# Optimization experiments

Hardware: AMD Instinct MI355X
Metric: run time of the kernel (lower is better)

Reference implementation:

```python
import jax, jax.numpy as jnp
import numpy as np

N, E, K, IN, OUT = 20000, 320000, 5, 256, 128
NAN_FRAC = 0.3


def setup_inputs() -> dict:
    key = jax.random.key(0)
    ks = jax.random.split(key, 8)
    x = jax.random.normal(ks[0], (N, IN), dtype=jnp.float32)
    nan_mask = jax.random.uniform(ks[1], (N, IN)) < NAN_FRAC
    x = jnp.where(nan_mask, jnp.nan, x)  # missing features as NaN
    edge_index = jax.random.randint(ks[2], (2, E), 0, N, dtype=jnp.int64)
    logp = jax.nn.log_softmax(jax.random.normal(ks[3], (K,), dtype=jnp.float32))
    means = jax.random.normal(ks[4], (K, IN), dtype=jnp.float32)
    logvars = jax.random.normal(ks[5], (K, IN), dtype=jnp.float32) * 0.1
    xav = 1.414 * np.sqrt(6.0 / (IN + OUT))
    weight = jax.random.uniform(ks[6], (IN, OUT), dtype=jnp.float32, minval=-xav, maxval=xav)
    bias = jnp.zeros((OUT,), dtype=jnp.float32)
    return {"x": x, "edge_index": edge_index, "logp": logp, "means": means,
            "logvars": logvars, "weight": weight, "bias": bias}


def _ex_relu(mu, sigma):
    # E[relu(X)] for X ~ N(mu, sigma); sigma is the variance
    sigma_s = jnp.where(sigma == 0, 1e-10, sigma)
    ss = jnp.sqrt(sigma_s)
    w = mu / ss
    nr = ss * (jnp.exp(-0.5 * w * w) / np.sqrt(2 * np.pi)
               + 0.5 * w * (1.0 + jax.lax.erf(w / np.sqrt(2))))
    return jnp.where(sigma == 0, jnp.maximum(mu, 0.0), nr)


def _gcn_norm(edge_index, num_nodes):
    # add self-loops, symmetric D^-1/2 A D^-1/2 normalization
    row = jnp.concatenate([edge_index[0], jnp.arange(num_nodes, dtype=edge_index.dtype)])
    col = jnp.concatenate([edge_index[1], jnp.arange(num_nodes, dtype=edge_index.dtype)])
    ones = jnp.ones(row.shape[0], dtype=jnp.float32)
    deg = jax.ops.segment_sum(ones, row, num_segments=num_nodes)
    dinv = jnp.where(deg > 0, jax.lax.rsqrt(deg), 0.0)
    wn = dinv[row] * dinv[col]
    return row, col, wn


def reference(x, edge_index, logp, means, logvars, weight, bias):
    n = x.shape[0]
    dim = x.shape[1]
    row, col, wn = _gcn_norm(edge_index, n)
    wn2 = wn * wn  # adj2 = adj * adj (elementwise on sparse values)

    isnan = jnp.isnan(x)                                       # [N, IN]
    variances = jnp.exp(logvars)                               # [K, IN]
    mean_mat = jnp.where(isnan[None], means[:, None, :], x[None])      # [K, N, IN]
    var_mat = jnp.where(isnan[None], variances[:, None, :], 0.0)       # [K, N, IN]

    transform_x = jnp.einsum('kni,io->kno', mean_mat, weight) + bias   # [K, N, OUT]
    transform_covs = jnp.einsum('kni,io->kno', var_mat, weight * weight)

    def spmm(vals, X):  # segment-sum SpMM: out[r] += vals_e * X[c]
        return jax.ops.segment_sum(X[col] * vals[:, None], row, num_segments=n)

    conv_x = jax.vmap(lambda X: spmm(wn, X))(transform_x)      # [K, N, OUT]
    conv_covs = jax.vmap(lambda X: spmm(wn2, X))(transform_covs)

    expected_x = _ex_relu(conv_x, conv_covs)                   # [K, N, OUT]

    # GMM responsibilities per node
    log_n = (-0.5 * jnp.sum((mean_mat - means[:, None, :]) ** 2 / variances[:, None, :], axis=2)
             - 0.5 * dim * np.log(2 * np.pi) - 0.5 * jnp.sum(logvars))  # [K, N]
    gamma = jax.nn.softmax(logp[:, None] + log_n, axis=0)      # [K, N]

    return jnp.sum(expected_x * gamma[:, :, None], axis=0)     # [N, OUT]
```

## Files before the change

kernel.cpp:

```cpp
#include <hip/hip_runtime.h>
#include <stdint.h>

#define N_NODES 20000
#define N_EDGES 320000
#define K_MIX 5
#define IN_F 256
#define OUT_F 128
#define NT 11

typedef __attribute__((ext_vector_type(8))) short short8;
typedef __attribute__((ext_vector_type(4))) float floatx4;

__device__ __forceinline__ float bf2f(unsigned int u) {
  union { unsigned int i; float f; } v;
  v.i = (u & 0xffffu) << 16;
  return v.f;
}
__device__ __forceinline__ unsigned short f2bf(float f) {
  union { float f; unsigned int i; } v;
  v.f = f;
  unsigned int x = v.i;
  unsigned int r = (x + 0x7fffu + ((x >> 16) & 1u)) >> 16;
  return (unsigned short)r;
}

__device__ __forceinline__ float exrelu(float mu, float sig) {
  if (sig < 1e-30f) return fmaxf(mu, 0.f);
  float ss = sqrtf(sig);
  float w = mu / ss;
  float e = __expf(-0.5f * w * w);
  float axv = fabsf(w) * 0.70710678118654752f;
  float t = 1.f / (1.f + 0.3275911f * axv);
  float poly = t * (0.254829592f +
              t * (-0.284496736f +
              t * (1.421413741f +
              t * (-1.453152027f + t * 1.061405429f))));
  float erfv = 1.f - poly * e;
  erfv = copysignf(erfv, w);
  return ss * (e * 0.3989422804014327f + 0.5f * w * (1.f + erfv));
}

__global__ void k_deg(const int* __restrict__ row, int* __restrict__ deg) {
  int t = blockIdx.x * 256 + threadIdx.x;
  if (t < N_EDGES) atomicAdd(&deg[row[t]], 1);
}

__global__ void k_scan1(const int* __restrict__ deg, int* __restrict__ startofs,
                        int* __restrict__ bsums, float* __restrict__ dinv) {
  __shared__ int sd[256];
  int t = threadIdx.x;
  int i = blockIdx.x * 256 + t;
  int v = (i < N_NODES) ? deg[i] : 0;
  if (i < N_NODES) dinv[i] = rsqrtf((float)(v + 1));
  sd[t] = v;
  __syncthreads();
  for (int off = 1; off < 256; off <<= 1) {
    int u = (t >= off) ? sd[t - off] : 0;
    __syncthreads();
    sd[t] += u;
    __syncthreads();
  }
  if (i < N_NODES) startofs[i] = sd[t] - v;
  if (t == 255) bsums[blockIdx.x] = sd[255];
}

__global__ void k_scan2(int* __restrict__ bsums, int nb) {
  __shared__ int sd[128];
  int t = threadIdx.x;
  int v = (t < nb) ? bsums[t] : 0;
  sd[t] = v;
  __syncthreads();
  for (int off = 1; off < 128; off <<= 1) {
    int u = (t >= off) ? sd[t - off] : 0;
    __syncthreads();
    sd[t] += u;
    __syncthreads();
  }
  if (t < nb) bsums[t] = sd[t] - v;
}

__global__ void k_scan3(int* __restrict__ startofs, int* __restrict__ cursor,
                        const int* __restrict__ bsums) {
  int i = blockIdx.x * 256 + threadIdx.x;
  if (i < N_NODES) {
    int s0 = startofs[i] + bsums[blockIdx.x];
    startofs[i] = s0;
    cursor[i] = s0;
  }
}

__global__ void k_scatter(const int* __restrict__ row, const int* __restrict__ col,
                          const float* __restrict__ dinv, int* __restrict__ cursor,
                          int* __restrict__ csr_col, float* __restrict__ csr_w) {
  int t = blockIdx.x * 256 + threadIdx.x;
  if (t < N_EDGES) {
    int r = row[t], c = col[t];
    int p = atomicAdd(&cursor[r], 1);
    csr_col[p] = c;
    csr_w[p] = dinv[r] * dinv[c];
  }
}

__global__ void k_buildB(const float* __restrict__ W, const float* __restrict__ means,
                         const float* __restrict__ logvars, unsigned short* __restrict__ Bt) {
  int idx = blockIdx.x * 256 + threadIdx.x;
  int j = idx >> 15;
  int rem = idx & 32767;
  int n = rem >> 8;
  int kk = rem & 255;
  float wv = W[kk * OUT_F + n];
  float val;
  if (j == 0) val = wv;
  else if (j <= 5) val = means[(j - 1) * IN_F + kk] * wv;
  else val = expf(logvars[(j - 6) * IN_F + kk]) * wv * wv;
  Bt[idx] = f2bf(val);
}

__global__ void k_prepx(const float* __restrict__ x, const float* __restrict__ logp,
                        const float* __restrict__ means, const float* __restrict__ logvars,
                        unsigned short* __restrict__ X0, float* __restrict__ gamma) {
  __shared__ float s_mean[K_MIX * IN_F];
  __shared__ float s_rv[K_MIX * IN_F];
  int t = threadIdx.x;
  for (int j = t; j < K_MIX * IN_F; j += 256) {
    s_mean[j] = means[j];
    s_rv[j] = expf(-logvars[j]);
  }
  __syncthreads();
  int node = blockIdx.x * 4 + (t >> 6);
  if (node >= N_NODES) return;
  int lane = t & 63;
  float4 xv = *(const float4*)(x + (size_t)node * IN_F + 4 * lane);
  float xf[4] = {xv.x, xv.y, xv.z, xv.w};
  float gsum[K_MIX] = {0, 0, 0, 0, 0};
  ushort4 o;
  unsigned short* op = (unsigned short*)&o;
#pragma unroll
  for (int j = 0; j < 4; j++) {
    bool nn = (xf[j] != xf[j]);
    op[j] = nn ? (unsigned short)0x7FC0 : f2bf(xf[j]);
    if (!nn) {
      int fi = 4 * lane + j;
#pragma unroll
      for (int k = 0; k < K_MIX; k++) {
        float d = xf[j] - s_mean[k * IN_F + fi];
        gsum[k] += d * d * s_rv[k * IN_F + fi];
      }
    }
  }
  *(ushort4*)(X0 + node * IN_F + 4 * lane) = o;
#pragma unroll
  for (int k = 0; k < K_MIX; k++)
    for (int off = 32; off; off >>= 1) gsum[k] += __shfl_xor(gsum[k], off, 64);
  if (lane == 0) {
    float lg[K_MIX], mx = -1e30f;
#pragma unroll
    for (int k = 0; k < K_MIX; k++) {
      lg[k] = logp[k] - 0.5f * gsum[k];
      mx = fmaxf(mx, lg[k]);
    }
    float se = 0.f;
#pragma unroll
    for (int k = 0; k < K_MIX; k++) { lg[k] = expf(lg[k] - mx); se += lg[k]; }
    float inv = 1.f / se;
#pragma unroll
    for (int k = 0; k < K_MIX; k++) gamma[node * K_MIX + k] = lg[k] * inv;
  }
}

__global__ __launch_bounds__(64) void k_spmm(const unsigned short* __restrict__ X0,
                       const int* __restrict__ startofs, const int* __restrict__ deg,
                       const float* __restrict__ dinv, const int* __restrict__ csr_col,
                       const float* __restrict__ csr_w, unsigned short* __restrict__ G,
                       float* __restrict__ sArr) {
  int node = blockIdx.x;
  int lane = threadIdx.x;
  int fo = 4 * lane;
  float ax[4] = {0, 0, 0, 0}, am[4] = {0, 0, 0, 0}, am2[4] = {0, 0, 0, 0};
  float ssum = 0.f;
  float ws = dinv[node];
  ws = ws * ws;
  int st = startofs[node];
  int total = deg[node] + 1;
  ushort4 zero4 = {0, 0, 0, 0};
  ushort4 B0 = zero4, B1 = zero4, B2 = zero4, B3 = zero4,
          B4 = zero4, B5 = zero4, B6 = zero4, B7 = zero4;
  float W0 = 0.f, W1 = 0.f, W2 = 0.f, W3 = 0.f,
        W4 = 0.f, W5 = 0.f, W6 = 0.f, W7 = 0.f;
  B0 = *(const ushort4*)(X0 + node * IN_F + fo); W0 = ws;
#define PFILL(S)                                                      \
  if (S < total) {                                                    \
    int c = csr_col[st + (S - 1)];                                    \
    W##S = csr_w[st + (S - 1)];                                       \
    B##S = *(const ushort4*)(X0 + c * IN_F + fo);                     \
  }
  PFILL(1) PFILL(2) PFILL(3) PFILL(4) PFILL(5) PFILL(6) PFILL(7)
#undef PFILL

#define STEP(S)                                                       \
  if (W##S != 0.f) {                                                  \
    float wv = W##S, wv2 = wv * wv;                                   \
    ssum += wv;                                                       \
    const unsigned short* xp = (const unsigned short*)&B##S;          \
    _Pragma("unroll")                                                 \
    for (int j = 0; j < 4; j++) {                                     \
      float xf = bf2f(xp[j]);                                         \
      bool nn = (xf != xf);                                           \
      ax[j] = fmaf(wv, nn ? 0.f : xf, ax[j]);                         \
      am[j] += nn ? wv : 0.f;                                         \
      am2[j] += nn ? wv2 : 0.f;                                       \
    }                                                                 \
  }                                                                   \
  if (base + 8 + S < total) {                                         \
    int c = csr_col[st + base + 7 + S];                               \
    W##S = csr_w[st + base + 7 + S];                                  \
    B##S = *(const ushort4*)(X0 + c * IN_F + fo);                     \
  } else {                                                            \
    W##S = 0.f;                                                       \
  }

  for (int base = 0; base < total; base += 8) {
    STEP(0) STEP(1) STEP(2) STEP(3) STEP(4) STEP(5) STEP(6) STEP(7)
  }
#undef STEP

  ushort4 o;
  o.x = f2bf(ax[0]); o.y = f2bf(ax[1]); o.z = f2bf(ax[2]); o.w = f2bf(ax[3]);
  *(ushort4*)(G + node * 768 + fo) = o;
  o.x = f2bf(am[0]); o.y = f2bf(am[1]); o.z = f2bf(am[2]); o.w = f2bf(am[3]);
  *(ushort4*)(G + node * 768 + 256 + fo) = o;
  o.x = f2bf(am2[0]); o.y = f2bf(am2[1]); o.z = f2bf(am2[2]); o.w = f2bf(am2[3]);
  *(ushort4*)(G + node * 768 + 512 + fo) = o;
  if (lane == 0) sArr[node] = ssum;
}

__global__ __launch_bounds__(256, 2) void k_gemm_ep(
    const unsigned short* __restrict__ G, const unsigned short* __restrict__ Bt,
    const float* __restrict__ gamma, const float* __restrict__ sArr,
    const float* __restrict__ bias, float* __restrict__ out) {
  __shared__ __align__(16) char A1ls[64 * 512];
  __shared__ __align__(16) char A2ls[64 * 512];
  __shared__ __align__(16) char Bls0[64 * 128];
  __shared__ __align__(16) char Bls1[64 * 128];
  int mt = blockIdx.x, ch = blockIdx.y;
  int t = threadIdx.x, wave = t >> 6, lane = t & 63;
  int wr = wave >> 1, wc = wave & 1;
  int quad = lane >> 4, l16 = lane & 15;

  floatx4 z = {0.f, 0.f, 0.f, 0.f};
  floatx4 cx[2][2], oa[2][2];
#pragma unroll
  for (int mi = 0; mi < 2; mi++)
#pragma unroll
    for (int ni = 0; ni < 2; ni++) { cx[mi][ni] = z; oa[mi][ni] = z; }

#define STAGE_A(dst, aoff_)                                              \
  {                                                                      \
    _Pragma("unroll")                                                    \
    for (int i = 0; i < 8; i++) {                                        \
      int f = i * 256 + t;                                               \
      int r = f >> 5, c = f & 31;                                        \
      int sw = c ^ (r & 7);                                              \
      int gr = mt * 64 + r;                                              \
      if (gr >= N_NODES) gr = N_NODES - 1;                               \
      *(uint4*)((dst) + r * 512 + sw * 16) =                             \
          *(const uint4*)(G + (size_t)gr * 768 + (aoff_) + c * 8);       \
    }                                                                    \
  }

#define STAGE_B(dst, jt_, k0_)                                           \
  {                                                                      \
    _Pragma("unroll")                                                    \
    for (int i = 0; i < 2; i++) {                                        \
      int f = i * 256 + t;                                               \
      int r = f >> 3, c = f & 7;                                         \
      int sw = c ^ (r & 7);                                              \
      *(uint4*)((dst) + r * 128 + sw * 16) =                             \
          *(const uint4*)(Bt + (size_t)(jt_)*32768 +                     \
                          (ch * 64 + r) * 256 + (k0_) + c * 8);          \
    }                                                                    \
  }

  STAGE_A(A1ls, 0)
  for (int k0 = 0; k0 < 256; k0 += 64) {
    __syncthreads();
    STAGE_B(Bls0, 0, k0)
    __syncthreads();
#pragma unroll
    for (int ks = 0; ks < 2; ks++) {
      int ccA = (k0 >> 3) + ks * 4 + quad;
      int ccB = ks * 4 + quad;
      short8 a[2], b[2];
#pragma unroll
      for (int mi = 0; mi < 2; mi++) {
        int r = wr * 32 + mi * 16 + l16;
        a[mi] = *(const short8*)(A1ls + r * 512 + (ccA ^ (r & 7)) * 16);
      }
#pragma unroll
      for (int ni = 0; ni < 2; ni++) {
        int r = wc * 32 + ni * 16 + l16;
        b[ni] = *(const short8*)(Bls0 + r * 128 + (ccB ^ (r & 7)) * 16);
      }
#pragma unroll
      for (int mi = 0; mi < 2; mi++)
#pragma unroll
        for (int ni = 0; ni < 2; ni++)
          cx[mi][ni] = __builtin_amdgcn_mfma_f32_16x16x32_bf16(a[mi], b[ni], cx[mi][ni], 0, 0, 0);
    }
  }

  __syncthreads();
  STAGE_A(A1ls, 256)
  STAGE_A(A2ls, 512)

  int gr0 = mt * 64 + wr * 32 + quad * 4;
  int gc0 = ch * 64 + wc * 32 + l16;
  float svr[2][4];
#pragma unroll
  for (int mi = 0; mi < 2; mi++)
#pragma unroll
    for (int reg = 0; reg < 4; reg++) {
      int gr = gr0 + mi * 16 + reg;
      if (gr >= N_NODES) gr = N_NODES - 1;
      svr[mi][reg] = sArr[gr];
    }
  float biasr[2] = {bias[gc0], bias[gc0 + 16]};

#pragma unroll 1
  for (int k = 0; k < K_MIX; k++) {
    floatx4 tm[2][2], tv[2][2];
#pragma unroll
    for (int mi = 0; mi < 2; mi++)
#pragma unroll
      for (int ni = 0; ni < 2; ni++) { tm[mi][ni] = z; tv[mi][ni] = z; }
    for (int k0 = 0; k0 < 256; k0 += 64) {
      __syncthreads();
      STAGE_B(Bls0, 1 + k, k0)
      STAGE_B(Bls1, 6 + k, k0)
      __syncthreads();
#pragma unroll
      for (int ks = 0; ks < 2; ks++) {
        int ccA = (k0 >> 3) + ks * 4 + quad;
        int ccB = ks * 4 + quad;
        short8 a1[2], a2[2], bm[2], bv[2];
#pragma unroll
        for (int mi = 0; mi < 2; mi++) {
          int r = wr * 32 + mi * 16 + l16;
          int sa = r * 512 + (ccA ^ (r & 7)) * 16;
          a1[mi] = *(const short8*)(A1ls + sa);
          a2[mi] = *(const short8*)(A2ls + sa);
        }
#pragma unroll
        for (int ni = 0; ni < 2; ni++) {
          int r = wc * 32 + ni * 16 + l16;
          int sb = r * 128 + (ccB ^ (r & 7)) * 16;
          bm[ni] = *(const short8*)(Bls0 + sb);
          bv[ni] = *(const short8*)(Bls1 + sb);
        }
#pragma unroll
        for (int mi = 0; mi < 2; mi++)
#pragma unroll
          for (int ni = 0; ni < 2; ni++) {
            tm[mi][ni] = __builtin_amdgcn_mfma_f32_16x16x32_bf16(a1[mi], bm[ni], tm[mi][ni], 0, 0, 0);
            tv[mi][ni] = __builtin_amdgcn_mfma_f32_16x16x32_bf16(a2[mi], bv[ni], tv[mi][ni], 0, 0, 0);
          }
      }
    }
#pragma unroll
    for (int mi = 0; mi < 2; mi++)
#pragma unroll
      for (int reg = 0; reg < 4; reg++) {
        int gr = gr0 + mi * 16 + reg;
        if (gr >= N_NODES) gr = N_NODES - 1;
        float g = gamma[gr * K_MIX + k];
#pragma unroll
        for (int ni = 0; ni < 2; ni++) {
          float mu = cx[mi][ni][reg] + tm[mi][ni][reg] + biasr[ni] * svr[mi][reg];
          oa[mi][ni][reg] += g * exrelu(mu, tv[mi][ni][reg]);
        }
      }
  }

#pragma unroll
  for (int mi = 0; mi < 2; mi++)
#pragma unroll
    for (int ni = 0; ni < 2; ni++)
#pragma unroll
      for (int reg = 0; reg < 4; reg++) {
        int gr = gr0 + mi * 16 + reg;
        if (gr < N_NODES) out[(size_t)gr * OUT_F + gc0 + ni * 16] = oa[mi][ni][reg];
      }
#undef STAGE_A
#undef STAGE_B
}

extern "C" void kernel_launch(void* const* d_in, const int* in_sizes, int n_in,
                              void* d_out, int out_size, void* d_ws, size_t ws_size,
                              hipStream_t stream) {
  const float* x = (const float*)d_in[0];
  const int* ei = (const int*)d_in[1];
  const float* logp = (const float*)d_in[2];
  const float* means = (const float*)d_in[3];
  const float* lvar = (const float*)d_in[4];
  const float* W = (const float*)d_in[5];
  const float* bias = (const float*)d_in[6];
  float* out = (float*)d_out;
  const int* row = ei;
  const int* col = ei + N_EDGES;

  char* p = (char*)d_ws;
  auto alloc = [&](size_t bytes) -> char* {
    char* q = p;
    p += (bytes + 255) & ~((size_t)255);
    return q;
  };
  int* deg = (int*)alloc(N_NODES * 4);
  float* dinv = (float*)alloc(N_NODES * 4);
  int* startofs = (int*)alloc(N_NODES * 4);
  int* cursor = (int*)alloc(N_NODES * 4);
  int* bsums = (int*)alloc(128 * 4);
  int* csr_col = (int*)alloc((size_t)N_EDGES * 4);
  float* csr_w = (float*)alloc((size_t)N_EDGES * 4);
  float* gamma = (float*)alloc((size_t)N_NODES * K_MIX * 4);
  float* sArr = (float*)alloc(N_NODES * 4);
  unsigned short* Bt = (unsigned short*)alloc((size_t)NT * 128 * 256 * 2);
  unsigned short* X0 = (unsigned short*)alloc((size_t)N_NODES * IN_F * 2);
  unsigned short* G = (unsigned short*)alloc((size_t)N_NODES * 768 * 2);

  hipMemsetAsync(deg, 0, N_NODES * 4, stream);
  k_deg<<<(N_EDGES + 255) / 256, 256, 0, stream>>>(row, deg);
  k_scan1<<<79, 256, 0, stream>>>(deg, startofs, bsums, dinv);
  k_scan2<<<1, 128, 0, stream>>>(bsums, 79);
  k_scan3<<<79, 256, 0, stream>>>(startofs, cursor, bsums);
  k_scatter<<<(N_EDGES + 255) / 256, 256, 0, stream>>>(row, col, dinv, cursor, csr_col, csr_w);
  k_buildB<<<(NT * 128 * 256) / 256, 256, 0, stream>>>(W, means, lvar, Bt);
  k_prepx<<<N_NODES / 4, 256, 0, stream>>>(x, logp, means, lvar, X0, gamma);
  k_spmm<<<N_NODES, 64, 0, stream>>>(X0, startofs, deg, dinv, csr_col, csr_w, G, sArr);
  k_gemm_ep<<<dim3((N_NODES + 63) / 64, 2), 256, 0, stream>>>(G, Bt, gamma, sArr, bias, out);
}
```

Before: 242.2 us.

## Pipeline GEMM B tiles via async global_load_lds into a triple-buffered ring

Rewrites the fused GEMM+epilogue kernel so all three A panels are staged up front using direct global-to-LDS loads, and B tiles flow through a 3-slot LDS ring prefetched with global_load_lds and gated by vmcnt waits. Gamma, scale and bias values are preloaded into shared memory once per block. This is meant to hide global memory latency behind MFMA work and remove the register round-trip of the old staging. In exchange LDS use rises to about 146KB, which likely cuts occupancy below the 2 blocks the launch bounds request. Correctness also depends on hand-tuned waitcnt counts.

New measurement: 284.8 us. +17.6%, slower.

```diff
diff --git a/kernel.cpp b/kernel.cpp
--- a/kernel.cpp
+++ b/kernel.cpp
@@ -38,6 +38,12 @@
   float erfv = 1.f - poly * e;
   erfv = copysignf(erfv, w);
   return ss * (e * 0.3989422804014327f + 0.5f * w * (1.f + erfv));
+}
+
+__device__ __forceinline__ void gll16(const void* g, void* l) {
+  __builtin_amdgcn_global_load_lds(
+      (const __attribute__((address_space(1))) void*)g,
+      (__attribute__((address_space(3))) void*)l, 16, 0, 0);
 }
 
 __global__ void k_deg(const int* __restrict__ row, int* __restrict__ deg) {
@@ -238,106 +244,120 @@
     const unsigned short* __restrict__ G, const unsigned short* __restrict__ Bt,
     const float* __restrict__ gamma, const float* __restrict__ sArr,
     const float* __restrict__ bias, float* __restrict__ out) {
-  __shared__ __align__(16) char A1ls[64 * 512];
-  __shared__ __align__(16) char A2ls[64 * 512];
-  __shared__ __align__(16) char Bls0[64 * 128];
-  __shared__ __align__(16) char Bls1[64 * 128];
+  __shared__ __align__(16) char A0ls[32768];
+  __shared__ __align__(16) char A1ls[32768];
+  __shared__ __align__(16) char A2ls[32768];
+  __shared__ __align__(16) char Bring[3 * 16384];
+  __shared__ float aux[448];
+
   int mt = blockIdx.x, ch = blockIdx.y;
-  int t = threadIdx.x, wave = t >> 6, lane = t & 63;
-  int wr = wave >> 1, wc = wave & 1;
-  int quad = lane >> 4, l16 = lane & 15;
+  int t = threadIdx.x, w = t >> 6, l = t & 63;
+  int wr = w >> 1, wc = w & 1;
+  int quad = l >> 4, l16 = l & 15;
+
+  for (int j = t; j < 448; j += 256) {
+    float v;
+    if (j < 320) {
+      int r = j / 5, k = j - r * 5;
+      int gr = mt * 64 + r; if (gr >= N_NODES) gr = N_NODES - 1;
+      v = gamma[gr * K_MIX + k];
+    } else if (j < 384) {
+      int gr = mt * 64 + (j - 320); if (gr >= N_NODES) gr = N_NODES - 1;
+      v = sArr[gr];
+    } else {
+      v = bias[ch * 64 + (j - 384)];
+    }
+    aux[j] = v;
+  }
+
+  {
+#pragma unroll
+    for (int s = 0; s < 3; s++) {
+      char* dst = (s == 0) ? A0ls : (s == 1) ? A1ls : A2ls;
+      int aoff = s * 256;
+#pragma unroll
+      for (int i = 0; i < 8; ++i) {
+        int r = i * 8 + w * 2 + (l >> 5);
+        int c = (l & 31) ^ (r & 7);
+        int gr = mt * 64 + r; if (gr >= N_NODES) gr = N_NODES - 1;
+        gll16(G + (size_t)gr * 768 + aoff + c * 8, dst + i * 4096 + w * 1024);
+      }
+    }
+  }
+
+#define ISSUE_B(qv, slotp)                                                \
+  {                                                                       \
+    int jm_, jv_, k0_;                                                    \
+    int q_ = (qv);                                                        \
+    if (q_ < 4) { jm_ = 0; jv_ = 0; k0_ = q_ * 64; }                      \
+    else { int qq_ = q_ - 4; int k_ = qq_ >> 2;                           \
+           jm_ = 1 + k_; jv_ = 6 + k_; k0_ = (qq_ & 3) * 64; }            \
+    int rb_ = w * 8 + (l >> 3);                                           \
+    int c8_ = ((l & 7) ^ ((l >> 3) & 7)) * 8;                             \
+    const unsigned short* bm_ =                                           \
+        Bt + jm_ * 32768 + (ch * 64 + rb_) * 256 + k0_ + c8_;             \
+    const unsigned short* bv_ =                                           \
+        Bt + jv_ * 32768 + (ch * 64 + rb_) * 256 + k0_ + c8_;             \
+    gll16(bm_, (slotp) + w * 1024);                                       \
+    gll16(bm_ + 32 * 256, (slotp) + 4096 + w * 1024);                     \
+    gll16(bv_, (slotp) + 8192 + w * 1024);                                \
+    gll16(bv_ + 32 * 256, (slotp) + 12288 + w * 1024);                    \
+  }
+
+  ISSUE_B(0, Bring)
+  ISSUE_B(1, Bring + 16384)
+  ISSUE_B(2, Bring + 32768)
+
+  asm volatile("s_waitcnt lgkmcnt(0)" ::: "memory");
 
   floatx4 z = {0.f, 0.f, 0.f, 0.f};
-  floatx4 cx[2][2], oa[2][2];
+  floatx4 cx[2][2], oa[2][2], tm[2][2], tv[2][2];
 #pragma unroll
   for (int mi = 0; mi < 2; mi++)
 #pragma unroll
     for (int ni = 0; ni < 2; ni++) { cx[mi][ni] = z; oa[mi][ni] = z; }
 
-#define STAGE_A(dst, aoff_)                                              \
-  {                                                                      \
-    _Pragma("unroll")                                                    \
-    for (int i = 0; i < 8; i++) {                                        \
-      int f = i * 256 + t;                                               \
-      int r = f >> 5, c = f & 31;                                        \
-      int sw = c ^ (r & 7);                                              \
-      int gr = mt * 64 + r;                                              \
-      if (gr >= N_NODES) gr = N_NODES - 1;                               \
-      *(uint4*)((dst) + r * 512 + sw * 16) =                             \
-          *(const uint4*)(G + (size_t)gr * 768 + (aoff_) + c * 8);       \
-    }                                                                    \
-  }
-
-#define STAGE_B(dst, jt_, k0_)                                           \
-  {                                                                      \
-    _Pragma("unroll")                                                    \
-    for (int i = 0; i < 2; i++) {                                        \
-      int f = i * 256 + t;                                               \
-      int r = f >> 3, c = f & 7;                                         \
-      int sw = c ^ (r & 7);                                              \
-      *(uint4*)((dst) + r * 128 + sw * 16) =                             \
-          *(const uint4*)(Bt + (size_t)(jt_)*32768 +                     \
-                          (ch * 64 + r) * 256 + (k0_) + c * 8);          \
-    }                                                                    \
-  }
-
-  STAGE_A(A1ls, 0)
-  for (int k0 = 0; k0 < 256; k0 += 64) {
-    __syncthreads();
-    STAGE_B(Bls0, 0, k0)
-    __syncthreads();
-#pragma unroll
-    for (int ks = 0; ks < 2; ks++) {
-      int ccA = (k0 >> 3) + ks * 4 + quad;
-      int ccB = ks * 4 + quad;
-      short8 a[2], b[2];
-#pragma unroll
-      for (int mi = 0; mi < 2; mi++) {
-        int r = wr * 32 + mi * 16 + l16;
-        a[mi] = *(const short8*)(A1ls + r * 512 + (ccA ^ (r & 7)) * 16);
-      }
-#pragma unroll
-      for (int ni = 0; ni < 2; ni++) {
-        int r = wc * 32 + ni * 16 + l16;
-        b[ni] = *(const short8*)(Bls0 + r * 128 + (ccB ^ (r & 7)) * 16);
-      }
-#pragma unroll
-      for (int mi = 0; mi < 2; mi++)
-#pragma unroll
-        for (int ni = 0; ni < 2; ni++)
-          cx[mi][ni] = __builtin_amdgcn_mfma_f32_16x16x32_bf16(a[mi], b[ni], cx[mi][ni], 0, 0, 0);
-    }
-  }
-
-  __syncthreads();
-  STAGE_A(A1ls, 256)
-  STAGE_A(A2ls, 512)
-
-  int gr0 = mt * 64 + wr * 32 + quad * 4;
-  int gc0 = ch * 64 + wc * 32 + l16;
-  float svr[2][4];
-#pragma unroll
-  for (int mi = 0; mi < 2; mi++)
-#pragma unroll
-    for (int reg = 0; reg < 4; reg++) {
-      int gr = gr0 + mi * 16 + reg;
-      if (gr >= N_NODES) gr = N_NODES - 1;
-      svr[mi][reg] = sArr[gr];
-    }
-  float biasr[2] = {bias[gc0], bias[gc0 + 16]};
-
-#pragma unroll 1
-  for (int k = 0; k < K_MIX; k++) {
-    floatx4 tm[2][2], tv[2][2];
-#pragma unroll
-    for (int mi = 0; mi < 2; mi++)
-#pragma unroll
-      for (int ni = 0; ni < 2; ni++) { tm[mi][ni] = z; tv[mi][ni] = z; }
-    for (int k0 = 0; k0 < 256; k0 += 64) {
-      __syncthreads();
-      STAGE_B(Bls0, 1 + k, k0)
-      STAGE_B(Bls1, 6 + k, k0)
-      __syncthreads();
+  for (int p = 0; p < 24; ++p) {
+    int sl = p - (p / 3) * 3;
+    char* slot = Bring + sl * 16384;
+
+    if (p < 22)       asm volatile("s_waitcnt vmcnt(8)" ::: "memory");
+    else if (p == 22) asm volatile("s_waitcnt vmcnt(4)" ::: "memory");
+    else              asm volatile("s_waitcnt vmcnt(0)" ::: "memory");
+    __builtin_amdgcn_s_barrier();
+
+    if (p < 4) {
+      int k0 = p * 64;
+#pragma unroll
+      for (int ks = 0; ks < 2; ks++) {
+        int ccA = (k0 >> 3) + ks * 4 + quad;
+        int ccB = ks * 4 + quad;
+        short8 a[2], b[2];
+#pragma unroll
+        for (int mi = 0; mi < 2; mi++) {
+          int r = wr * 32 + mi * 16 + l16;
+          a[mi] = *(const short8*)(A0ls + r * 512 + (ccA ^ (r & 7)) * 16);
+        }
+#pragma unroll
+        for (int ni = 0; ni < 2; ni++) {
+          int r = wc * 32 + ni * 16 + l16;
+          b[ni] = *(const short8*)(slot + r * 128 + (ccB ^ (r & 7)) * 16);
+        }
+#pragma unroll
+        for (int mi = 0; mi < 2; mi++)
+#pragma unroll
+          for (int ni = 0; ni < 2; ni++)
+            cx[mi][ni] = __builtin_amdgcn_mfma_f32_16x16x32_bf16(a[mi], b[ni], cx[mi][ni], 0, 0, 0);
+      }
+    } else {
+      int q = p - 4;
+      int k0 = (q & 3) * 64;
+      if ((q & 3) == 0) {
+#pragma unroll
+        for (int mi = 0; mi < 2; mi++)
+#pragma unroll
+          for (int ni = 0; ni < 2; ni++) { tm[mi][ni] = z; tv[mi][ni] = z; }
+      }
 #pragma unroll
       for (int ks = 0; ks < 2; ks++) {
         int ccA = (k0 >> 3) + ks * 4 + quad;
@@ -354,8 +374,8 @@
         for (int ni = 0; ni < 2; ni++) {
           int r = wc * 32 + ni * 16 + l16;
           int sb = r * 128 + (ccB ^ (r & 7)) * 16;
-          bm[ni] = *(const short8*)(Bls0 + sb);
-          bv[ni] = *(const short8*)(Bls1 + sb);
+          bm[ni] = *(const short8*)(slot + sb);
+          bv[ni] = *(const short8*)(slot + 8192 + sb);
         }
 #pragma unroll
         for (int mi = 0; mi < 2; mi++)
@@ -365,22 +385,35 @@
             tv[mi][ni] = __builtin_amdgcn_mfma_f32_16x16x32_bf16(a2[mi], bv[ni], tv[mi][ni], 0, 0, 0);
           }
       }
+      if ((q & 3) == 3) {
+        int kk = q >> 2;
+#pragma unroll
+        for (int mi = 0; mi < 2; mi++)
+#pragma unroll
+          for (int reg = 0; reg < 4; reg++) {
+            int row = wr * 32 + mi * 16 + quad * 4 + reg;
+            float g = aux[row * 5 + kk];
+            float sv = aux[320 + row];
+#pragma unroll
+            for (int ni = 0; ni < 2; ni++) {
+              float bia = aux[384 + wc * 32 + ni * 16 + l16];
+              float mu = cx[mi][ni][reg] + tm[mi][ni][reg] + bia * sv;
+              oa[mi][ni][reg] += g * exrelu(mu, tv[mi][ni][reg]);
+            }
+          }
+      }
     }
-#pragma unroll
-    for (int mi = 0; mi < 2; mi++)
-#pragma unroll
-      for (int reg = 0; reg < 4; reg++) {
-        int gr = gr0 + mi * 16 + reg;
-        if (gr >= N_NODES) gr = N_NODES - 1;
-        float g = gamma[gr * K_MIX + k];
-#pragma unroll
-        for (int ni = 0; ni < 2; ni++) {
-          float mu = cx[mi][ni][reg] + tm[mi][ni][reg] + biasr[ni] * svr[mi][reg];
-          oa[mi][ni][reg] += g * exrelu(mu, tv[mi][ni][reg]);
-        }
-      }
-  }
-
+
+    asm volatile("s_waitcnt lgkmcnt(0)" ::: "memory");
+    __builtin_amdgcn_s_barrier();
+    if (p + 3 < 24) ISSUE_B(p + 3, slot)
+  }
+#undef ISSUE_B
+
+  asm volatile("s_waitcnt vmcnt(0)" ::: "memory");
+
+  int gr0 = mt * 64 + wr * 32 + quad * 4;
+  int gc0 = ch * 64 + wc * 32 + l16;
 #pragma unroll
   for (int mi = 0; mi < 2; mi++)
 #pragma unroll
@@ -390,8 +423,6 @@
         int gr = gr0 + mi * 16 + reg;
         if (gr < N_NODES) out[(size_t)gr * OUT_F + gc0 + ni * 16] = oa[mi][ni][reg];
       }
-#undef STAGE_A
-#undef STAGE_B
 }
 
 extern "C" void kernel_launch(void* const* d_in, const int* in_sizes, int n_in,
```

## Load GEMM B fragments directly from global and stage A via global_load_lds

Applied to the files above, without the earlier changes.

The fused GEMM+epilogue kernel stops staging the weight (B) tiles through LDS and instead has each lane read its MFMA B fragment straight from global memory, which removes two barriers per k-step in every mixture-component loop. The A tiles are now copied with the global_load_lds direct-to-LDS builtin, and gamma, sArr and bias are preloaded into a small shared aux array. The goal is to cut LDS traffic and synchronisation, at the cost of more uncoalesced global/L2 reads of B per wave.

New measurement: 259.0 us. +6.9%, slower.

```diff
diff --git a/kernel.cpp b/kernel.cpp
--- a/kernel.cpp
+++ b/kernel.cpp
@@ -38,6 +38,12 @@
   float erfv = 1.f - poly * e;
   erfv = copysignf(erfv, w);
   return ss * (e * 0.3989422804014327f + 0.5f * w * (1.f + erfv));
+}
+
+__device__ __forceinline__ void gll16(const void* g, void* l) {
+  __builtin_amdgcn_global_load_lds(
+      (const __attribute__((address_space(1))) void*)g,
+      (__attribute__((address_space(3))) void*)l, 16, 0, 0);
 }
 
 __global__ void k_deg(const int* __restrict__ row, int* __restrict__ deg) {
@@ -238,58 +244,60 @@
     const unsigned short* __restrict__ G, const unsigned short* __restrict__ Bt,
     const float* __restrict__ gamma, const float* __restrict__ sArr,
     const float* __restrict__ bias, float* __restrict__ out) {
-  __shared__ __align__(16) char A1ls[64 * 512];
-  __shared__ __align__(16) char A2ls[64 * 512];
-  __shared__ __align__(16) char Bls0[64 * 128];
-  __shared__ __align__(16) char Bls1[64 * 128];
+  __shared__ __align__(16) char A1ls[32768];
+  __shared__ __align__(16) char A2ls[32768];
+  __shared__ float aux[448];
+
   int mt = blockIdx.x, ch = blockIdx.y;
-  int t = threadIdx.x, wave = t >> 6, lane = t & 63;
-  int wr = wave >> 1, wc = wave & 1;
-  int quad = lane >> 4, l16 = lane & 15;
-
-  floatx4 z = {0.f, 0.f, 0.f, 0.f};
-  floatx4 cx[2][2], oa[2][2];
-#pragma unroll
-  for (int mi = 0; mi < 2; mi++)
-#pragma unroll
-    for (int ni = 0; ni < 2; ni++) { cx[mi][ni] = z; oa[mi][ni] = z; }
+  int t = threadIdx.x, w = t >> 6, l = t & 63;
+  int wr = w >> 1, wc = w & 1;
+  int quad = l >> 4, l16 = l & 15;
+
+  for (int j = t; j < 448; j += 256) {
+    float v;
+    if (j < 320) {
+      int r = j / 5, k = j - r * 5;
+      int gr = mt * 64 + r; if (gr >= N_NODES) gr = N_NODES - 1;
+      v = gamma[gr * K_MIX + k];
+    } else if (j < 384) {
+      int gr = mt * 64 + (j - 320); if (gr >= N_NODES) gr = N_NODES - 1;
+      v = sArr[gr];
+    } else {
+      v = bias[ch * 64 + (j - 384)];
+    }
+    aux[j] = v;
+  }
 
 #define STAGE_A(dst, aoff_)                                              \
   {                                                                      \
     _Pragma("unroll")                                                    \
-    for (int i = 0; i < 8; i++) {                                        \
-      int f = i * 256 + t;                                               \
-      int r = f >> 5, c = f & 31;                                        \
-      int sw = c ^ (r & 7);                                              \
-      int gr = mt * 64 + r;                                              \
-      if (gr >= N_NODES) gr = N_NODES - 1;                               \
-      *(uint4*)((dst) + r * 512 + sw * 16) =                             \
-          *(const uint4*)(G + (size_t)gr * 768 + (aoff_) + c * 8);       \
+    for (int i = 0; i < 8; ++i) {                                        \
+      int r = i * 8 + w * 2 + (l >> 5);                                  \
+      int c = (l & 31) ^ (r & 7);                                        \
+      int gr = mt * 64 + r; if (gr >= N_NODES) gr = N_NODES - 1;         \
+      gll16(G + (size_t)gr * 768 + (aoff_) + c * 8,                      \
+            (dst) + i * 4096 + w * 1024);                                \
     }                                                                    \
   }
 
-#define STAGE_B(dst, jt_, k0_)                                           \
-  {                                                                      \
-    _Pragma("unroll")                                                    \
-    for (int i = 0; i < 2; i++) {                                        \
-      int f = i * 256 + t;                                               \
-      int r = f >> 3, c = f & 7;                                         \
-      int sw = c ^ (r & 7);                                              \
-      *(uint4*)((dst) + r * 128 + sw * 16) =                             \
-          *(const uint4*)(Bt + (size_t)(jt_)*32768 +                     \
-                          (ch * 64 + r) * 256 + (k0_) + c * 8);          \
-    }                                                                    \
-  }
-
   STAGE_A(A1ls, 0)
+  __syncthreads();
+
+  const unsigned short* Bp = Bt + ((size_t)(ch * 64 + wc * 32 + l16)) * 256;
+
+  floatx4 z = {0.f, 0.f, 0.f, 0.f};
+  floatx4 cx[2][2], oa[2][2];
+#pragma unroll
+  for (int mi = 0; mi < 2; mi++)
+#pragma unroll
+    for (int ni = 0; ni < 2; ni++) { cx[mi][ni] = z; oa[mi][ni] = z; }
+
+#pragma unroll
   for (int k0 = 0; k0 < 256; k0 += 64) {
-    __syncthreads();
-    STAGE_B(Bls0, 0, k0)
-    __syncthreads();
 #pragma unroll
     for (int ks = 0; ks < 2; ks++) {
       int ccA = (k0 >> 3) + ks * 4 + quad;
-      int ccB = ks * 4 + quad;
+      int kel = k0 + ks * 32 + quad * 8;
       short8 a[2], b[2];
 #pragma unroll
       for (int mi = 0; mi < 2; mi++) {
@@ -297,10 +305,8 @@
         a[mi] = *(const short8*)(A1ls + r * 512 + (ccA ^ (r & 7)) * 16);
       }
 #pragma unroll
-      for (int ni = 0; ni < 2; ni++) {
-        int r = wc * 32 + ni * 16 + l16;
-        b[ni] = *(const short8*)(Bls0 + r * 128 + (ccB ^ (r & 7)) * 16);
-      }
+      for (int ni = 0; ni < 2; ni++)
+        b[ni] = *(const short8*)(Bp + ni * 4096 + kel);
 #pragma unroll
       for (int mi = 0; mi < 2; mi++)
 #pragma unroll
@@ -312,36 +318,23 @@
   __syncthreads();
   STAGE_A(A1ls, 256)
   STAGE_A(A2ls, 512)
-
-  int gr0 = mt * 64 + wr * 32 + quad * 4;
-  int gc0 = ch * 64 + wc * 32 + l16;
-  float svr[2][4];
-#pragma unroll
-  for (int mi = 0; mi < 2; mi++)
-#pragma unroll
-    for (int reg = 0; reg < 4; reg++) {
-      int gr = gr0 + mi * 16 + reg;
-      if (gr >= N_NODES) gr = N_NODES - 1;
-      svr[mi][reg] = sArr[gr];
-    }
-  float biasr[2] = {bias[gc0], bias[gc0 + 16]};
+  __syncthreads();
 
 #pragma unroll 1
   for (int k = 0; k < K_MIX; k++) {
+    const unsigned short* Bm = Bp + (size_t)(1 + k) * 32768;
+    const unsigned short* Bv = Bp + (size_t)(6 + k) * 32768;
     floatx4 tm[2][2], tv[2][2];
 #pragma unroll
     for (int mi = 0; mi < 2; mi++)
 #pragma unroll
       for (int ni = 0; ni < 2; ni++) { tm[mi][ni] = z; tv[mi][ni] = z; }
+#pragma unroll
     for (int k0 = 0; k0 < 256; k0 += 64) {
-      __syncthreads();
-      STAGE_B(Bls0, 1 + k, k0)
-      STAGE_B(Bls1, 6 + k, k0)
-      __syncthreads();
 #pragma unroll
       for (int ks = 0; ks < 2; ks++) {
         int ccA = (k0 >> 3) + ks * 4 + quad;
-        int ccB = ks * 4 + quad;
+        int kel = k0 + ks * 32 + quad * 8;
         short8 a1[2], a2[2], bm[2], bv[2];
 #pragma unroll
         for (int mi = 0; mi < 2; mi++) {
@@ -352,10 +345,8 @@
         }
 #pragma unroll
         for (int ni = 0; ni < 2; ni++) {
-          int r = wc * 32 + ni * 16 + l16;
-          int sb = r * 128 + (ccB ^ (r & 7)) * 16;
-          bm[ni] = *(const short8*)(Bls0 + sb);
-          bv[ni] = *(const short8*)(Bls1 + sb);
+          bm[ni] = *(const short8*)(Bm + ni * 4096 + kel);
+          bv[ni] = *(const short8*)(Bv + ni * 4096 + kel);
         }
 #pragma unroll
         for (int mi = 0; mi < 2; mi++)
@@ -370,17 +361,20 @@
     for (int mi = 0; mi < 2; mi++)
 #pragma unroll
       for (int reg = 0; reg < 4; reg++) {
-        int gr = gr0 + mi * 16 + reg;
-        if (gr >= N_NODES) gr = N_NODES - 1;
-        float g = gamma[gr * K_MIX + k];
+        int row = wr * 32 + mi * 16 + quad * 4 + reg;
+        float g = aux[row * 5 + k];
+        float sv = aux[320 + row];
 #pragma unroll
         for (int ni = 0; ni < 2; ni++) {
-          float mu = cx[mi][ni][reg] + tm[mi][ni][reg] + biasr[ni] * svr[mi][reg];
+          float bia = aux[384 + wc * 32 + ni * 16 + l16];
+          float mu = cx[mi][ni][reg] + tm[mi][ni][reg] + bia * sv;
           oa[mi][ni][reg] += g * exrelu(mu, tv[mi][ni][reg]);
         }
       }
   }
 
+  int gr0 = mt * 64 + wr * 32 + quad * 4;
+  int gc0 = ch * 64 + wc * 32 + l16;
 #pragma unroll
   for (int mi = 0; mi < 2; mi++)
 #pragma unroll
@@ -391,7 +385,6 @@
         if (gr < N_NODES) out[(size_t)gr * OUT_F + gc0 + ni * 16] = oa[mi][ni][reg];
       }
 #undef STAGE_A
-#undef STAGE_B
 }
 
 extern "C" void kernel_launch(void* const* d_in, const int* in_sizes, int n_in,
```
